# Kernel tuning notes

Hardware: AMD Instinct MI355X
Metric: run time of the kernel (lower is better)

Reference implementation:

```python
import jax, jax.numpy as jnp
import numpy as np

B, C, H, W = 256, 256, 14, 14
CH = C // 2  # 128
N = H * W    # 196
EPS = 1e-5


def setup_inputs() -> dict:
    key = jax.random.key(0)
    ks = jax.random.split(key, 8)
    return {
        "x": jax.random.normal(ks[0], (B, C, H, W), jnp.float32),
        "y": jax.random.normal(ks[1], (B, C, H, W), jnp.float32),
        "Wq": jax.random.normal(ks[2], (CH, C), jnp.float32) * 0.05,
        "Wk": jax.random.normal(ks[3], (CH, C), jnp.float32) * 0.05,
        "Wv": jax.random.normal(ks[4], (CH, C), jnp.float32) * 0.05,
        "Wz": jax.random.normal(ks[5], (C, CH), jnp.float32) * 0.05,
        "bn_weight": jnp.ones((C,), jnp.float32),
        "bn_bias": jnp.zeros((C,), jnp.float32),
        "bn_mean": jax.random.normal(ks[6], (C,), jnp.float32) * 0.1,
        "bn_var": jax.random.uniform(ks[7], (C,), jnp.float32, 0.5, 1.5),
    }


def reference(x, y, Wq, Wk, Wv, Wz, bn_weight, bn_bias, bn_mean, bn_var):
    b = x.shape[0]
    xf = x.reshape(b, C, N)  # [B, C, N]
    yf = y.reshape(b, C, N)
    # 1x1 convs == channel matmuls
    Q = jnp.einsum('oc,bcn->bon', Wq, xf)  # [B, CH, N]
    K = jnp.einsum('oc,bcn->bon', Wk, yf)
    V = jnp.einsum('oc,bcn->bon', Wv, yf)
    # M = Q^T K  -> [B, N, N]
    M = jnp.einsum('bcq,bck->bqk', Q, K)
    # Softmax2d over a singleton channel dim (faithful to original: yields ones)
    M = jax.nn.softmax(M[:, None, :, :], axis=1)[:, 0]
    Z = jnp.einsum('bcn,bnm->bcm', V, M)  # [B, CH, N]
    Z = jnp.einsum('oc,bcn->bon', Wz, Z)  # [B, C, N]
    Z = Z.reshape(b, C, H, W)
    # BatchNorm2d (inference form with running stats)
    inv = jax.lax.rsqrt(bn_var + EPS)
    Z = (Z - bn_mean[:, None, None]) * (inv * bn_weight)[:, None, None] + bn_bias[:, None, None]
    return x + Z
```

## Files before the change

kernel.cpp:

```cpp
#include <hip/hip_runtime.h>
#include <hip/hip_bf16.h>

#define B_  256
#define C_  256
#define CH_ 128
#define N_  196
#define NF4 49
#define EPS 1e-5f

__global__ __launch_bounds__(256) void k_ysum(const float* __restrict__ y,
                                              float* __restrict__ ysum) {
    int wave = blockIdx.x * 4 + (threadIdx.x >> 6);
    int lane = threadIdx.x & 63;
    const float4* row = (const float4*)(y + (size_t)wave * N_);
    float s = 0.f;
    if (lane < NF4) {
        float4 v = row[lane];
        s = (v.x + v.y) + (v.z + v.w);
    }
    #pragma unroll
    for (int off = 32; off > 0; off >>= 1)
        s += __shfl_down(s, off, 64);
    if (lane == 0) ysum[wave] = s;
}

__global__ __launch_bounds__(256) void k_wzvt(const float* __restrict__ Wz,
                                              const float* __restrict__ Wv,
                                              float* __restrict__ WzvT) {
    __shared__ float sWv[CH_];
    int c = blockIdx.x;
    int o = threadIdx.x;
    if (o < CH_) sWv[o] = Wv[o * C_ + c];
    __syncthreads();
    const float4* wzrow = (const float4*)(Wz + o * CH_);
    float acc = 0.f;
    #pragma unroll
    for (int k4 = 0; k4 < CH_ / 4; k4++) {
        float4 w = wzrow[k4];
        acc += w.x * sWv[4 * k4 + 0];
        acc += w.y * sWv[4 * k4 + 1];
        acc += w.z * sWv[4 * k4 + 2];
        acc += w.w * sWv[4 * k4 + 3];
    }
    WzvT[c * C_ + o] = acc;
}

__global__ __launch_bounds__(256) void k_z2(const float* __restrict__ ysum,
                                            const float* __restrict__ WzvT,
                                            const float* __restrict__ bnw,
                                            const float* __restrict__ bnb,
                                            const float* __restrict__ bnm,
                                            const float* __restrict__ bnv,
                                            float* __restrict__ Zs) {
    __shared__ float sY[C_];
    int b = blockIdx.x;
    int o = threadIdx.x;
    sY[o] = ysum[b * C_ + o];
    __syncthreads();
    float acc = 0.f;
    #pragma unroll 8
    for (int c = 0; c < C_; c++)
        acc += sY[c] * WzvT[c * C_ + o];
    float alpha = bnw[o] * rsqrtf(bnv[o] + EPS);
    Zs[b * C_ + o] = (acc - bnm[o]) * alpha + bnb[o];
}

__global__ __launch_bounds__(256) void k_out(const float* __restrict__ x,
                                             const float* __restrict__ Zs,
                                             float* __restrict__ out) {
    int idx = blockIdx.x * blockDim.x + threadIdx.x;
    int row = idx / NF4;
    float z = Zs[row];
    float4 v = ((const float4*)x)[idx];
    v.x += z; v.y += z; v.z += z; v.w += z;
    ((float4*)out)[idx] = v;
}

extern "C" void kernel_launch(void* const* d_in, const int* in_sizes, int n_in,
                              void* d_out, int out_size, void* d_ws, size_t ws_size,
                              hipStream_t stream) {
    const float* x   = (const float*)d_in[0];
    const float* y   = (const float*)d_in[1];
    const float* Wv  = (const float*)d_in[4];
    const float* Wz  = (const float*)d_in[5];
    const float* bnw = (const float*)d_in[6];
    const float* bnb = (const float*)d_in[7];
    const float* bnm = (const float*)d_in[8];
    const float* bnv = (const float*)d_in[9];
    float* out = (float*)d_out;

    float* ysum = (float*)d_ws;
    float* WzvT = ysum + B_ * C_;
    float* Zs   = WzvT + C_ * C_;

    k_ysum<<<(B_ * C_) / 4, 256, 0, stream>>>(y, ysum);
    k_wzvt<<<C_, 256, 0, stream>>>(Wz, Wv, WzvT);
    k_z2<<<B_, 256, 0, stream>>>(ysum, WzvT, bnw, bnb, bnm, bnv, Zs);
    k_out<<<(B_ * C_ * NF4) / 256, 256, 0, stream>>>(x, Zs, out);
}
```

Before: 171.1 us.

## Fuse y-sum, channel matvec, BN and residual add into one per-batch kernel

Replaces three kernels (y spatial sum, z matvec, residual add) with a single kernel that uses one 1024-thread block per batch. The block reduces y rows into shared memory, runs the 256x256 matvec split across four segments, and adds the result to x. BN scaling is folded into the precomputed WzvT matrix. This removes intermediate global round-trips and launch gaps, but only 256 blocks cover the whole GPU, which limits memory-level parallelism for the streaming x read and out write.

New measurement: 167.3 us. -2.2%, faster.

```diff
diff --git a/kernel.cpp b/kernel.cpp
--- a/kernel.cpp
+++ b/kernel.cpp
@@ -1,32 +1,18 @@
 #include <hip/hip_runtime.h>
-#include <hip/hip_bf16.h>
 
-#define B_  256
-#define C_  256
-#define CH_ 128
-#define N_  196
-#define NF4 49
-#define EPS 1e-5f
-
-__global__ __launch_bounds__(256) void k_ysum(const float* __restrict__ y,
-                                              float* __restrict__ ysum) {
-    int wave = blockIdx.x * 4 + (threadIdx.x >> 6);
-    int lane = threadIdx.x & 63;
-    const float4* row = (const float4*)(y + (size_t)wave * N_);
-    float s = 0.f;
-    if (lane < NF4) {
-        float4 v = row[lane];
-        s = (v.x + v.y) + (v.z + v.w);
-    }
-    #pragma unroll
-    for (int off = 32; off > 0; off >>= 1)
-        s += __shfl_down(s, off, 64);
-    if (lane == 0) ysum[wave] = s;
-}
+#define B_   256
+#define C_   256
+#define CH_  128
+#define N_   196
+#define NF4  49
+#define NROW4 12544
+#define EPS  1e-5f
 
 __global__ __launch_bounds__(256) void k_wzvt(const float* __restrict__ Wz,
                                               const float* __restrict__ Wv,
-                                              float* __restrict__ WzvT) {
+                                              const float* __restrict__ bnw,
+                                              const float* __restrict__ bnv,
+                                              float* __restrict__ WzvTs) {
     __shared__ float sWv[CH_];
     int c = blockIdx.x;
     int o = threadIdx.x;
@@ -42,38 +28,89 @@
         acc += w.z * sWv[4 * k4 + 2];
         acc += w.w * sWv[4 * k4 + 3];
     }
-    WzvT[c * C_ + o] = acc;
+    float alpha = bnw[o] * rsqrtf(bnv[o] + EPS);
+    WzvTs[c * C_ + o] = acc * alpha;
 }
 
-__global__ __launch_bounds__(256) void k_z2(const float* __restrict__ ysum,
-                                            const float* __restrict__ WzvT,
-                                            const float* __restrict__ bnw,
-                                            const float* __restrict__ bnb,
-                                            const float* __restrict__ bnm,
-                                            const float* __restrict__ bnv,
-                                            float* __restrict__ Zs) {
+__global__ __launch_bounds__(1024, 4) void k_main(const float* __restrict__ x,
+                                                  const float* __restrict__ y,
+                                                  const float* __restrict__ WzvTs,
+                                                  const float* __restrict__ bnw,
+                                                  const float* __restrict__ bnb,
+                                                  const float* __restrict__ bnm,
+                                                  const float* __restrict__ bnv,
+                                                  float* __restrict__ out) {
     __shared__ float sY[C_];
-    int b = blockIdx.x;
-    int o = threadIdx.x;
-    sY[o] = ysum[b * C_ + o];
+    __shared__ float sPart[4][C_];
+    __shared__ float sZ[C_];
+
+    int b    = blockIdx.x;
+    int tid  = threadIdx.x;
+    int w    = tid >> 6;
+    int lane = tid & 63;
+
+    const float4* yb = (const float4*)y + (size_t)b * NROW4;
+    #pragma unroll
+    for (int i = 0; i < 16; i += 4) {
+        float s[4];
+        #pragma unroll
+        for (int j = 0; j < 4; j++) {
+            int r = (w << 4) + i + j;
+            float4 v = make_float4(0.f, 0.f, 0.f, 0.f);
+            if (lane < NF4) v = yb[r * NF4 + lane];
+            s[j] = (v.x + v.y) + (v.z + v.w);
+        }
+        #pragma unroll
+        for (int off = 32; off > 0; off >>= 1) {
+            #pragma unroll
+            for (int j = 0; j < 4; j++) s[j] += __shfl_down(s[j], off, 64);
+        }
+        if (lane == 0) {
+            #pragma unroll
+            for (int j = 0; j < 4; j++) sY[(w << 4) + i + j] = s[j];
+        }
+    }
     __syncthreads();
-    float acc = 0.f;
-    #pragma unroll 8
-    for (int c = 0; c < C_; c++)
-        acc += sY[c] * WzvT[c * C_ + o];
-    float alpha = bnw[o] * rsqrtf(bnv[o] + EPS);
-    Zs[b * C_ + o] = (acc - bnm[o]) * alpha + bnb[o];
-}
 
-__global__ __launch_bounds__(256) void k_out(const float* __restrict__ x,
-                                             const float* __restrict__ Zs,
-                                             float* __restrict__ out) {
-    int idx = blockIdx.x * blockDim.x + threadIdx.x;
-    int row = idx / NF4;
-    float z = Zs[row];
-    float4 v = ((const float4*)x)[idx];
-    v.x += z; v.y += z; v.z += z; v.w += z;
-    ((float4*)out)[idx] = v;
+    {
+        int o   = tid & (C_ - 1);
+        int seg = tid >> 8;
+        int c0  = seg * 64;
+        float acc = 0.f;
+        #pragma unroll 8
+        for (int c = 0; c < 64; c++)
+            acc += sY[c0 + c] * WzvTs[(c0 + c) * C_ + o];
+        sPart[seg][o] = acc;
+    }
+    __syncthreads();
+    if (tid < C_) {
+        float z = sPart[0][tid] + sPart[1][tid] + sPart[2][tid] + sPart[3][tid];
+        float alpha = bnw[tid] * rsqrtf(bnv[tid] + EPS);
+        sZ[tid] = z + bnb[tid] - bnm[tid] * alpha;
+    }
+    __syncthreads();
+
+    const float4* xb = (const float4*)x   + (size_t)b * NROW4;
+    float4*       ob = (float4*)out       + (size_t)b * NROW4;
+    #pragma unroll
+    for (int k = 0; k < 12; k++) {
+        int idx = tid + (k << 10);
+        int r = idx / NF4;
+        float z = sZ[r];
+        float4 v = xb[idx];
+        v.x += z; v.y += z; v.z += z; v.w += z;
+        ob[idx] = v;
+    }
+    {
+        int idx = tid + (12 << 10);
+        if (idx < NROW4) {
+            int r = idx / NF4;
+            float z = sZ[r];
+            float4 v = xb[idx];
+            v.x += z; v.y += z; v.z += z; v.w += z;
+            ob[idx] = v;
+        }
+    }
 }
 
 extern "C" void kernel_launch(void* const* d_in, const int* in_sizes, int n_in,
@@ -89,12 +126,8 @@
     const float* bnv = (const float*)d_in[9];
     float* out = (float*)d_out;
 
-    float* ysum = (float*)d_ws;
-    float* WzvT = ysum + B_ * C_;
-    float* Zs   = WzvT + C_ * C_;
+    float* WzvTs = (float*)d_ws;
 
-    k_ysum<<<(B_ * C_) / 4, 256, 0, stream>>>(y, ysum);
-    k_wzvt<<<C_, 256, 0, stream>>>(Wz, Wv, WzvT);
-    k_z2<<<B_, 256, 0, stream>>>(ysum, WzvT, bnw, bnb, bnm, bnv, Zs);
-    k_out<<<(B_ * C_ * NF4) / 256, 256, 0, stream>>>(x, Zs, out);
+    k_wzvt<<<C_, 256, 0, stream>>>(Wz, Wv, bnw, bnv, WzvTs);
+    k_main<<<B_, 1024, 0, stream>>>(x, y, WzvTs, bnw, bnb, bnm, bnv, out);
 }
```
